# Performance work log

Hardware: AMD Instinct MI355X
Metric: run time of the kernel (lower is better)

Reference implementation:

```python
import jax, jax.numpy as jnp
import numpy as np

N_NODES = 1048576
N_GRAPHS = 4096
NODES_PER_GRAPH = N_NODES // N_GRAPHS
N_EDGES = 8388608
F_IN = 16
HID = 32


def _glorot(k, shp):
    return jax.random.normal(k, shp, jnp.float32) * np.float32(np.sqrt(2.0 / (shp[-2] + shp[-1])))


def setup_inputs() -> dict:
    key = jax.random.key(0)
    ks = jax.random.split(key, 8)
    d = F_IN + HID  # DCRNN gate convs act on cat([X, H])
    return {
        "x": jax.random.normal(ks[0], (N_NODES, F_IN), jnp.float32),
        "edge_index": jax.random.randint(ks[1], (2, N_EDGES), 0, N_NODES),
        "edge_weight": jax.random.uniform(ks[2], (N_EDGES,), jnp.float32),
        "batch": jnp.repeat(jnp.arange(N_GRAPHS), NODES_PER_GRAPH),
        "W_z": _glorot(ks[3], (2, 1, d, HID)),
        "b_z": jnp.zeros((HID,), jnp.float32),
        "W_r": _glorot(ks[4], (2, 1, d, HID)),
        "b_r": jnp.zeros((HID,), jnp.float32),
        "W_h": _glorot(ks[5], (2, 1, d, HID)),
        "b_h": jnp.zeros((HID,), jnp.float32),
        "W_lin": _glorot(ks[6], (HID, 1)),
        "b_lin": jnp.zeros((1,), jnp.float32),
    }


def _dconv_k1(X, W, b):
    # torch_geometric_temporal DConv with K=1: the diffusion loop never runs,
    # so H = X @ W[0,0] + X @ W[1,0] + b (edge_index/edge_weight unused).
    return X @ (W[0, 0] + W[1, 0]) + b


def reference(x, edge_index, edge_weight, batch, W_z, b_z, W_r, b_r, W_h, b_h, W_lin, b_lin):
    del edge_index, edge_weight  # mathematically unused when K=1
    h0 = jnp.zeros((x.shape[0], HID), x.dtype)  # DCRNN hidden state default
    xh = jnp.concatenate([x, h0], axis=1)
    Z = jax.nn.sigmoid(_dconv_k1(xh, W_z, b_z))
    R = jax.nn.sigmoid(_dconv_k1(xh, W_r, b_r))
    xhr = jnp.concatenate([x, h0 * R], axis=1)
    H_tilde = jnp.tanh(_dconv_k1(xhr, W_h, b_h))
    H = Z * h0 + (1.0 - Z) * H_tilde  # (N, 32)
    h = jax.nn.relu(H)
    h = h @ W_lin + b_lin  # (N, 1)
    # global_mean_pool over per-node graph ids
    sums = jax.ops.segment_sum(h, batch, num_segments=N_GRAPHS)
    cnts = jax.ops.segment_sum(jnp.ones((h.shape[0], 1), h.dtype), batch, num_segments=N_GRAPHS)
    return sums / jnp.maximum(cnts, 1.0)  # (N_GRAPHS, 1)
```

## Files before the change

### kernel.cpp

```cpp
#include <hip/hip_runtime.h>

#define N_GRAPHS  4096
#define NPG       256
#define F_IN      16
#define HID       32
#define LOG2E     1.4426950408889634f

typedef _Float16 half8  __attribute__((ext_vector_type(8)));
typedef float    f32x16 __attribute__((ext_vector_type(16)));

#if __has_builtin(__builtin_amdgcn_exp2f)
#define EXP2(x) __builtin_amdgcn_exp2f(x)
#else
#define EXP2(x) exp2f(x)
#endif

typedef const __attribute__((address_space(1))) void* gptr_t;
typedef __attribute__((address_space(3))) void*       lptr_t;

__device__ __forceinline__ float gate_term(float az, float ah, float wl, float osum)
{
    const float e1 = EXP2(az);
    const float e2 = EXP2(fminf(ah, 126.0f));
    const float r  = __builtin_amdgcn_rcpf((1.0f + e1) * (e2 + 1.0f));
    float v = (e2 - 1.0f) * r;
    v = v > 0.0f ? v : 0.0f;
    return fmaf(v, wl, osum);
}

__device__ __forceinline__ float tile32(float4 c0, float4 c1,
    half8 Bz, half8 Bh, float bzl, float bhl, float wll, float osum)
{
    const float xf[8] = { c0.x, c0.y, c0.z, c0.w, c1.x, c1.y, c1.z, c1.w };
    half8 Ah, Al;
#pragma unroll
    for (int j = 0; j < 8; ++j) {
        const _Float16 h = (_Float16)xf[j];
        Ah[j] = h;
        Al[j] = (_Float16)(xf[j] - (float)h);
    }
    f32x16 accZ, accH;
#pragma unroll
    for (int i = 0; i < 16; ++i) { accZ[i] = bzl; accH[i] = bhl; }
    accZ = __builtin_amdgcn_mfma_f32_32x32x16_f16(Ah, Bz, accZ, 0, 0, 0);
    accH = __builtin_amdgcn_mfma_f32_32x32x16_f16(Ah, Bh, accH, 0, 0, 0);
    accZ = __builtin_amdgcn_mfma_f32_32x32x16_f16(Al, Bz, accZ, 0, 0, 0);
    accH = __builtin_amdgcn_mfma_f32_32x32x16_f16(Al, Bh, accH, 0, 0, 0);
#pragma unroll
    for (int i = 0; i < 16; ++i)
        osum = gate_term(accZ[i], accH[i], wll, osum);
    return osum;
}

__global__ __launch_bounds__(256, 4) void gcn_fused(
    const float* __restrict__ x,
    const float* __restrict__ Wz, const float* __restrict__ bz,
    const float* __restrict__ Wh, const float* __restrict__ bh,
    const float* __restrict__ Wlin, const float* __restrict__ blin,
    float* __restrict__ out)
{
    __shared__ __attribute__((aligned(16))) float xs[4 * 2048];
    __shared__ float part[4];
    const int t = threadIdx.x, wv = t >> 6, lane = t & 63;
    const int col = lane & 31, p = lane >> 5;
    const int g = blockIdx.x * 2 + (wv >> 1), half = wv & 1;
    float* xs_wave = xs + wv * 2048;

    float z0[8], z1[8], h0[8], h1[8];
#pragma unroll
    for (int j = 0; j < 8; ++j) {
        const int k = p * 8 + j;
        z0[j] = Wz[k * 32 + col];
        z1[j] = Wz[1536 + k * 32 + col];
        h0[j] = Wh[k * 32 + col];
        h1[j] = Wh[1536 + k * 32 + col];
    }
    const float bz_raw = bz[col], bh_raw = bh[col];
    const float wll = Wlin[col], bl = blin[0];
    __builtin_amdgcn_sched_barrier(0);

    const int gu = col * 16 + p * 8;
    const float* gbase = x + ((size_t)g * NPG + half * 128) * F_IN;
#pragma unroll
    for (int tau = 0; tau < 4; ++tau) {
        const float* src = gbase + tau * 512 + gu;
        __builtin_amdgcn_global_load_lds((gptr_t)src,
                                         (lptr_t)(xs_wave + tau * 512), 16, 0, 0);
        __builtin_amdgcn_global_load_lds((gptr_t)(src + 4),
                                         (lptr_t)(xs_wave + tau * 512 + 256), 16, 0, 0);
    }
    __builtin_amdgcn_sched_barrier(0);

    half8 Bz, Bh;
#pragma unroll
    for (int j = 0; j < 8; ++j) {
        Bz[j] = (_Float16)((z0[j] + z1[j]) * LOG2E);
        Bh[j] = (_Float16)((h0[j] + h1[j]) * (2.0f * LOG2E));
    }
    const float bzl = bz_raw * LOG2E;
    const float bhl = bh_raw * (2.0f * LOG2E);

    float osum = 0.0f;

    asm volatile("s_waitcnt vmcnt(6)" ::: "memory");
    {
        const float4 c0 = *(const float4*)(xs_wave + 0 * 512 + lane * 4);
        const float4 c1 = *(const float4*)(xs_wave + 0 * 512 + 256 + lane * 4);
        osum = tile32(c0, c1, Bz, Bh, bzl, bhl, wll, osum);
    }
    asm volatile("s_waitcnt vmcnt(4)" ::: "memory");
    {
        const float4 c0 = *(const float4*)(xs_wave + 1 * 512 + lane * 4);
        const float4 c1 = *(const float4*)(xs_wave + 1 * 512 + 256 + lane * 4);
        osum = tile32(c0, c1, Bz, Bh, bzl, bhl, wll, osum);
    }
    asm volatile("s_waitcnt vmcnt(2)" ::: "memory");
    {
        const float4 c0 = *(const float4*)(xs_wave + 2 * 512 + lane * 4);
        const float4 c1 = *(const float4*)(xs_wave + 2 * 512 + 256 + lane * 4);
        osum = tile32(c0, c1, Bz, Bh, bzl, bhl, wll, osum);
    }
    asm volatile("s_waitcnt vmcnt(0)" ::: "memory");
    {
        const float4 c0 = *(const float4*)(xs_wave + 3 * 512 + lane * 4);
        const float4 c1 = *(const float4*)(xs_wave + 3 * 512 + 256 + lane * 4);
        osum = tile32(c0, c1, Bz, Bh, bzl, bhl, wll, osum);
    }

#pragma unroll
    for (int off = 32; off > 0; off >>= 1)
        osum += __shfl_down(osum, off, 64);

    if (lane == 0) part[wv] = osum;
    __syncthreads();
    if (t == 0) {
        out[blockIdx.x * 2]     = (part[0] + part[1]) * (1.0f / (float)NPG) + bl;
        out[blockIdx.x * 2 + 1] = (part[2] + part[3]) * (1.0f / (float)NPG) + bl;
    }
}

extern "C" void kernel_launch(void* const* d_in, const int* in_sizes, int n_in,
                              void* d_out, int out_size, void* d_ws, size_t ws_size,
                              hipStream_t stream)
{
    const float* x    = (const float*)d_in[0];
    const float* Wz   = (const float*)d_in[4];
    const float* bz   = (const float*)d_in[5];
    const float* Wh   = (const float*)d_in[8];
    const float* bh   = (const float*)d_in[9];
    const float* Wlin = (const float*)d_in[10];
    const float* blin = (const float*)d_in[11];
    float* out = (float*)d_out;
    (void)d_ws; (void)ws_size;

    gcn_fused<<<N_GRAPHS / 2, 256, 0, stream>>>(x, Wz, bz, Wh, bh, Wlin, blin, out);
}
```

Measured before the change: 166.7 us.

## Give each wave two whole graphs with double-buffered LDS staging

Each wave now handles two full graphs (four 128-node half-tiles) rather than half a graph. It stages them through a two-slot LDS double buffer, so the next half's loads are in flight while the current one is computed. Because a wave owns whole graphs, the cross-wave LDS reduction and __syncthreads disappear and each wave writes its own two outputs. The cost is a larger LDS footprint (64KB per block), lower launch_bounds occupancy, and a quarter as many blocks, which may reduce how much latency can be hidden across waves.

```diff
diff --git a/kernel.cpp b/kernel.cpp
--- a/kernel.cpp
+++ b/kernel.cpp
@@ -52,19 +52,40 @@
     return osum;
 }
 
-__global__ __launch_bounds__(256, 4) void gcn_fused(
+#define STAGE(hgi, bufofs) do {                                               \
+    _Pragma("unroll")                                                         \
+    for (int tau = 0; tau < 4; ++tau) {                                       \
+        const float* src_ = xw_base + (hgi) * 2048 + tau * 512 + gu;          \
+        __builtin_amdgcn_global_load_lds((gptr_t)src_,                        \
+            (lptr_t)(xs_wave + (bufofs) + tau * 512), 16, 0, 0);              \
+        __builtin_amdgcn_global_load_lds((gptr_t)(src_ + 4),                  \
+            (lptr_t)(xs_wave + (bufofs) + tau * 512 + 256), 16, 0, 0);        \
+        __builtin_amdgcn_sched_barrier(0);                                    \
+    }                                                                         \
+} while (0)
+
+#define TILE_AT(bufofs, tau, NW, ACC) do {                                    \
+    asm volatile("s_waitcnt vmcnt(" #NW ")" ::: "memory");                    \
+    __builtin_amdgcn_sched_barrier(0);                                        \
+    const float4 c0_ = *(const float4*)(xs_wave + (bufofs) + (tau) * 512 + lane * 4);        \
+    const float4 c1_ = *(const float4*)(xs_wave + (bufofs) + (tau) * 512 + 256 + lane * 4);  \
+    ACC = tile32(c0_, c1_, Bz, Bh, bzl, bhl, wll, ACC);                       \
+} while (0)
+
+__global__ __launch_bounds__(256, 2) void gcn_fused(
     const float* __restrict__ x,
     const float* __restrict__ Wz, const float* __restrict__ bz,
     const float* __restrict__ Wh, const float* __restrict__ bh,
     const float* __restrict__ Wlin, const float* __restrict__ blin,
     float* __restrict__ out)
 {
-    __shared__ __attribute__((aligned(16))) float xs[4 * 2048];
-    __shared__ float part[4];
+    __shared__ __attribute__((aligned(16))) float xs[4 * 4096];
     const int t = threadIdx.x, wv = t >> 6, lane = t & 63;
     const int col = lane & 31, p = lane >> 5;
-    const int g = blockIdx.x * 2 + (wv >> 1), half = wv & 1;
-    float* xs_wave = xs + wv * 2048;
+    const int wave_id = blockIdx.x * 4 + wv;
+    float* xs_wave = xs + wv * 4096;
+    const float* xw_base = x + (size_t)wave_id * 8192;
+    const int gu = col * 16 + p * 8;
 
     float z0[8], z1[8], h0[8], h1[8];
 #pragma unroll
@@ -79,17 +100,8 @@
     const float wll = Wlin[col], bl = blin[0];
     __builtin_amdgcn_sched_barrier(0);
 
-    const int gu = col * 16 + p * 8;
-    const float* gbase = x + ((size_t)g * NPG + half * 128) * F_IN;
-#pragma unroll
-    for (int tau = 0; tau < 4; ++tau) {
-        const float* src = gbase + tau * 512 + gu;
-        __builtin_amdgcn_global_load_lds((gptr_t)src,
-                                         (lptr_t)(xs_wave + tau * 512), 16, 0, 0);
-        __builtin_amdgcn_global_load_lds((gptr_t)(src + 4),
-                                         (lptr_t)(xs_wave + tau * 512 + 256), 16, 0, 0);
-    }
-    __builtin_amdgcn_sched_barrier(0);
+    STAGE(0, 0);
+    STAGE(1, 2048);
 
     half8 Bz, Bh;
 #pragma unroll
@@ -100,42 +112,32 @@
     const float bzl = bz_raw * LOG2E;
     const float bhl = bh_raw * (2.0f * LOG2E);
 
-    float osum = 0.0f;
+    float osA = 0.0f, osB = 0.0f;
 
-    asm volatile("s_waitcnt vmcnt(6)" ::: "memory");
-    {
-        const float4 c0 = *(const float4*)(xs_wave + 0 * 512 + lane * 4);
-        const float4 c1 = *(const float4*)(xs_wave + 0 * 512 + 256 + lane * 4);
-        osum = tile32(c0, c1, Bz, Bh, bzl, bhl, wll, osum);
-    }
-    asm volatile("s_waitcnt vmcnt(4)" ::: "memory");
-    {
-        const float4 c0 = *(const float4*)(xs_wave + 1 * 512 + lane * 4);
-        const float4 c1 = *(const float4*)(xs_wave + 1 * 512 + 256 + lane * 4);
-        osum = tile32(c0, c1, Bz, Bh, bzl, bhl, wll, osum);
-    }
-    asm volatile("s_waitcnt vmcnt(2)" ::: "memory");
-    {
-        const float4 c0 = *(const float4*)(xs_wave + 2 * 512 + lane * 4);
-        const float4 c1 = *(const float4*)(xs_wave + 2 * 512 + 256 + lane * 4);
-        osum = tile32(c0, c1, Bz, Bh, bzl, bhl, wll, osum);
-    }
-    asm volatile("s_waitcnt vmcnt(0)" ::: "memory");
-    {
-        const float4 c0 = *(const float4*)(xs_wave + 3 * 512 + lane * 4);
-        const float4 c1 = *(const float4*)(xs_wave + 3 * 512 + 256 + lane * 4);
-        osum = tile32(c0, c1, Bz, Bh, bzl, bhl, wll, osum);
-    }
+    TILE_AT(0, 0, 14, osA); TILE_AT(0, 1, 12, osA);
+    TILE_AT(0, 2, 10, osA); TILE_AT(0, 3,  8, osA);
+    STAGE(2, 0);
+
+    TILE_AT(2048, 0, 14, osA); TILE_AT(2048, 1, 12, osA);
+    TILE_AT(2048, 2, 10, osA); TILE_AT(2048, 3,  8, osA);
+    STAGE(3, 2048);
+
+    TILE_AT(0, 0, 14, osB); TILE_AT(0, 1, 12, osB);
+    TILE_AT(0, 2, 10, osB); TILE_AT(0, 3,  8, osB);
+
+    TILE_AT(2048, 0, 6, osB); TILE_AT(2048, 1, 4, osB);
+    TILE_AT(2048, 2, 2, osB); TILE_AT(2048, 3, 0, osB);
 
 #pragma unroll
-    for (int off = 32; off > 0; off >>= 1)
-        osum += __shfl_down(osum, off, 64);
-
-    if (lane == 0) part[wv] = osum;
-    __syncthreads();
-    if (t == 0) {
-        out[blockIdx.x * 2]     = (part[0] + part[1]) * (1.0f / (float)NPG) + bl;
-        out[blockIdx.x * 2 + 1] = (part[2] + part[3]) * (1.0f / (float)NPG) + bl;
+    for (int off = 32; off > 0; off >>= 1) {
+        osA += __shfl_down(osA, off, 64);
+        osB += __shfl_down(osB, off, 64);
+    }
+    if (lane == 0) {
+        float2 o;
+        o.x = osA * (1.0f / (float)NPG) + bl;
+        o.y = osB * (1.0f / (float)NPG) + bl;
+        *(float2*)(out + wave_id * 2) = o;
     }
 }
 
@@ -153,5 +155,5 @@
     float* out = (float*)d_out;
     (void)d_ws; (void)ws_size;
 
-    gcn_fused<<<N_GRAPHS / 2, 256, 0, stream>>>(x, Wz, bz, Wh, bh, Wlin, blin, out);
+    gcn_fused<<<N_GRAPHS / 8, 256, 0, stream>>>(x, Wz, bz, Wh, bh, Wlin, blin, out);
 }
```

Result: slower. 190.9 us (+14.5%).

## Assign one graph per wave with double-buffered LDS staging of node chunks

Applied to the files above, without the earlier changes.

Each wave now processes a whole graph, streaming four 64-node chunks through two LDS buffers with vmcnt/lgkmcnt fences instead of loading its half-graph in one shot. This removes the cross-wave LDS partial reduction and __syncthreads, and halves the block count. Weight loads are now waited on before x staging begins, which serializes their latency in front of the first global loads.

```diff
diff --git a/kernel.cpp b/kernel.cpp
--- a/kernel.cpp
+++ b/kernel.cpp
@@ -52,6 +52,32 @@
     return osum;
 }
 
+#define STAGE_CHUNK(cidx, bufofs) do {                                        \
+    const float* s_ = gb + (cidx) * 1024 + gu;                                \
+    __builtin_amdgcn_global_load_lds((gptr_t)(s_),                            \
+        (lptr_t)(xsw + (bufofs)),       16, 0, 0);                            \
+    __builtin_amdgcn_global_load_lds((gptr_t)(s_ + 4),                        \
+        (lptr_t)(xsw + (bufofs) + 256), 16, 0, 0);                            \
+    __builtin_amdgcn_global_load_lds((gptr_t)(s_ + 512),                      \
+        (lptr_t)(xsw + (bufofs) + 512), 16, 0, 0);                            \
+    __builtin_amdgcn_global_load_lds((gptr_t)(s_ + 516),                      \
+        (lptr_t)(xsw + (bufofs) + 768), 16, 0, 0);                            \
+    __builtin_amdgcn_sched_barrier(0);                                        \
+} while (0)
+
+#define COMPUTE_CHUNK(bufofs, NW) do {                                        \
+    asm volatile("s_waitcnt vmcnt(" #NW ")" ::: "memory");                    \
+    __builtin_amdgcn_sched_barrier(0);                                        \
+    { const float4 c0_ = *(const float4*)(xsw + (bufofs) + lane * 4);         \
+      const float4 c1_ = *(const float4*)(xsw + (bufofs) + 256 + lane * 4);   \
+      osum = tile32(c0_, c1_, Bz, Bh, bzl, bhl, wll, osum); }                 \
+    { const float4 c0_ = *(const float4*)(xsw + (bufofs) + 512 + lane * 4);   \
+      const float4 c1_ = *(const float4*)(xsw + (bufofs) + 768 + lane * 4);   \
+      osum = tile32(c0_, c1_, Bz, Bh, bzl, bhl, wll, osum); }                 \
+} while (0)
+
+#define RESTAGE_FENCE() asm volatile("s_waitcnt lgkmcnt(0)" ::: "memory")
+
 __global__ __launch_bounds__(256, 4) void gcn_fused(
     const float* __restrict__ x,
     const float* __restrict__ Wz, const float* __restrict__ bz,
@@ -60,83 +86,44 @@
     float* __restrict__ out)
 {
     __shared__ __attribute__((aligned(16))) float xs[4 * 2048];
-    __shared__ float part[4];
     const int t = threadIdx.x, wv = t >> 6, lane = t & 63;
     const int col = lane & 31, p = lane >> 5;
-    const int g = blockIdx.x * 2 + (wv >> 1), half = wv & 1;
-    float* xs_wave = xs + wv * 2048;
-
-    float z0[8], z1[8], h0[8], h1[8];
-#pragma unroll
-    for (int j = 0; j < 8; ++j) {
-        const int k = p * 8 + j;
-        z0[j] = Wz[k * 32 + col];
-        z1[j] = Wz[1536 + k * 32 + col];
-        h0[j] = Wh[k * 32 + col];
-        h1[j] = Wh[1536 + k * 32 + col];
-    }
-    const float bz_raw = bz[col], bh_raw = bh[col];
-    const float wll = Wlin[col], bl = blin[0];
-    __builtin_amdgcn_sched_barrier(0);
-
+    const int g = blockIdx.x * 4 + wv;
+    float* xsw = xs + wv * 2048;
+    const float* gb = x + (size_t)g * (NPG * F_IN);
     const int gu = col * 16 + p * 8;
-    const float* gbase = x + ((size_t)g * NPG + half * 128) * F_IN;
-#pragma unroll
-    for (int tau = 0; tau < 4; ++tau) {
-        const float* src = gbase + tau * 512 + gu;
-        __builtin_amdgcn_global_load_lds((gptr_t)src,
-                                         (lptr_t)(xs_wave + tau * 512), 16, 0, 0);
-        __builtin_amdgcn_global_load_lds((gptr_t)(src + 4),
-                                         (lptr_t)(xs_wave + tau * 512 + 256), 16, 0, 0);
-    }
-    __builtin_amdgcn_sched_barrier(0);
 
     half8 Bz, Bh;
 #pragma unroll
     for (int j = 0; j < 8; ++j) {
-        Bz[j] = (_Float16)((z0[j] + z1[j]) * LOG2E);
-        Bh[j] = (_Float16)((h0[j] + h1[j]) * (2.0f * LOG2E));
+        const int k = p * 8 + j;
+        Bz[j] = (_Float16)((Wz[k * 32 + col] + Wz[1536 + k * 32 + col]) * LOG2E);
+        Bh[j] = (_Float16)((Wh[k * 32 + col] + Wh[1536 + k * 32 + col]) * (2.0f * LOG2E));
     }
-    const float bzl = bz_raw * LOG2E;
-    const float bhl = bh_raw * (2.0f * LOG2E);
+    const float bzl = bz[col] * LOG2E;
+    const float bhl = bh[col] * (2.0f * LOG2E);
+    const float wll = Wlin[col], bl = blin[0];
+
+    asm volatile("s_waitcnt vmcnt(0)" ::: "memory");
+    __builtin_amdgcn_sched_barrier(0);
 
     float osum = 0.0f;
-
-    asm volatile("s_waitcnt vmcnt(6)" ::: "memory");
-    {
-        const float4 c0 = *(const float4*)(xs_wave + 0 * 512 + lane * 4);
-        const float4 c1 = *(const float4*)(xs_wave + 0 * 512 + 256 + lane * 4);
-        osum = tile32(c0, c1, Bz, Bh, bzl, bhl, wll, osum);
-    }
-    asm volatile("s_waitcnt vmcnt(4)" ::: "memory");
-    {
-        const float4 c0 = *(const float4*)(xs_wave + 1 * 512 + lane * 4);
-        const float4 c1 = *(const float4*)(xs_wave + 1 * 512 + 256 + lane * 4);
-        osum = tile32(c0, c1, Bz, Bh, bzl, bhl, wll, osum);
-    }
-    asm volatile("s_waitcnt vmcnt(2)" ::: "memory");
-    {
-        const float4 c0 = *(const float4*)(xs_wave + 2 * 512 + lane * 4);
-        const float4 c1 = *(const float4*)(xs_wave + 2 * 512 + 256 + lane * 4);
-        osum = tile32(c0, c1, Bz, Bh, bzl, bhl, wll, osum);
-    }
-    asm volatile("s_waitcnt vmcnt(0)" ::: "memory");
-    {
-        const float4 c0 = *(const float4*)(xs_wave + 3 * 512 + lane * 4);
-        const float4 c1 = *(const float4*)(xs_wave + 3 * 512 + 256 + lane * 4);
-        osum = tile32(c0, c1, Bz, Bh, bzl, bhl, wll, osum);
-    }
+    STAGE_CHUNK(0, 0);
+    STAGE_CHUNK(1, 1024);
+    COMPUTE_CHUNK(0, 4);
+    RESTAGE_FENCE();
+    STAGE_CHUNK(2, 0);
+    COMPUTE_CHUNK(1024, 4);
+    RESTAGE_FENCE();
+    STAGE_CHUNK(3, 1024);
+    COMPUTE_CHUNK(0, 4);
+    COMPUTE_CHUNK(1024, 0);
 
 #pragma unroll
     for (int off = 32; off > 0; off >>= 1)
         osum += __shfl_down(osum, off, 64);
-
-    if (lane == 0) part[wv] = osum;
-    __syncthreads();
-    if (t == 0) {
-        out[blockIdx.x * 2]     = (part[0] + part[1]) * (1.0f / (float)NPG) + bl;
-        out[blockIdx.x * 2 + 1] = (part[2] + part[3]) * (1.0f / (float)NPG) + bl;
-    }
+    if (lane == 0)
+        out[g] = osum * (1.0f / (float)NPG) + bl;
 }
 
 extern "C" void kernel_launch(void* const* d_in, const int* in_sizes, int n_in,
@@ -153,5 +140,5 @@
     float* out = (float*)d_out;
     (void)d_ws; (void)ws_size;
 
-    gcn_fused<<<N_GRAPHS / 2, 256, 0, stream>>>(x, Wz, bz, Wh, bh, Wlin, blin, out);
+    gcn_fused<<<N_GRAPHS / 4, 256, 0, stream>>>(x, Wz, bz, Wh, bh, Wlin, blin, out);
 }
```

Measured after the change: 171.3 us. +2.8%, slower.
